# Optimization experiments

Measured on AMD Instinct MI355X. Metric: run time of the kernel, lower is better.

The kernel has to match this reference:

```python
import jax, jax.numpy as jnp
import numpy as np

N_LINEARS = 16
CHANNELS = 3
OUTPUT_DIM = 64
Z_DIM = 128
BATCH = 512


def hash_vectors(z, n):
    # Deterministic surrogate for repo's hash_vectors: map each latent vector
    # to an integer bucket in [0, n). Data-dependent, jit-compatible.
    s = jnp.abs(jnp.sum(z, axis=1)) * 1000.0
    return jnp.mod(jnp.floor(s).astype(jnp.int32), n)


def setup_inputs() -> dict:
    key = jax.random.key(0)
    k1, k2, k3 = jax.random.split(key, 3)
    out_features = CHANNELS * OUTPUT_DIM ** 2 * N_LINEARS  # 196608
    z = jax.random.normal(k1, (BATCH, Z_DIM), dtype=jnp.float32)
    # Linear weight stored as (out_features, in_features), torch convention.
    W = jax.random.normal(k2, (out_features, Z_DIM), dtype=jnp.float32) * (1.0 / np.sqrt(Z_DIM))
    b = jax.random.normal(k3, (out_features,), dtype=jnp.float32) * 0.01
    return {"z": z, "W": W, "b": b}


def reference(z, W, b):
    B = z.shape[0]
    # Dense GEMM: (B, out_features)
    out = jnp.einsum('bi,oi->bo', z, W) + b
    out = out.reshape(B, N_LINEARS, CHANNELS, OUTPUT_DIM, OUTPUT_DIM)
    c = hash_vectors(z, N_LINEARS)  # (B,) int32 in [0, N_LINEARS)
    # Per-sample gather of one linear's output block.
    return jnp.take_along_axis(out, c[:, None, None, None, None], axis=1)[:, 0]
```

## Files before the change

### kernel.cpp

```cpp
#include <hip/hip_runtime.h>
#include <hip/hip_bf16.h>
#include <math.h>


#define N_LINEARS 16
#define ZD 128
#define BATCH 512
#define BLOCK_OUT 12288
#define STILE 48
#define SLOTS 64
#define ZROWS (ZD + 1)
#define TJ 256

typedef float vf16 __attribute__((ext_vector_type(16)));
typedef vf16 vf16u __attribute__((aligned(16)));

#define LISTS_OFF 16
#define BP_OFF (36864 / 4)
#define ZG_OFF_BYTES 65536

__global__ __launch_bounds__(512) void hash_kernel(
    const float* __restrict__ z, int* __restrict__ counts,
    int* __restrict__ lists, int* __restrict__ bp) {
  __shared__ int cnt[N_LINEARS];
  const int b = threadIdx.x;
  if (b < N_LINEARS) cnt[b] = 0;
  __syncthreads();

  const float* zr = z + b * ZD;
  float r0 = zr[0], r1 = zr[1], r2 = zr[2], r3 = zr[3];
  float r4 = zr[4], r5 = zr[5], r6 = zr[6], r7 = zr[7];
  #pragma unroll
  for (int i = 8; i < ZD; i += 8) {
    r0 += zr[i + 0]; r1 += zr[i + 1]; r2 += zr[i + 2]; r3 += zr[i + 3];
    r4 += zr[i + 4]; r5 += zr[i + 5]; r6 += zr[i + 6]; r7 += zr[i + 7];
  }
  float res = ((r0 + r1) + (r2 + r3)) + ((r4 + r5) + (r6 + r7));
  float v = fabsf(res) * 1000.0f;
  int cb = ((int)floorf(v)) & (N_LINEARS - 1);

  int pos = atomicAdd(&cnt[cb], 1);
  lists[(cb << 9) + pos] = b;
  bp[b] = cb | (pos << 4);

  __syncthreads();
  if (b < N_LINEARS) counts[b] = cnt[b];
}

__global__ __launch_bounds__(128) void gather_kernel(
    const float* __restrict__ z, const int* __restrict__ bp,
    float* __restrict__ zgT) {
  const int b = blockIdx.x;
  const int k = threadIdx.x;
  const int v = bp[b];
  const int cb = v & 15;
  const int pos = v >> 4;
  if (pos < SLOTS)
    zgT[(size_t)cb * (ZROWS * SLOTS) + (size_t)k * SLOTS + pos] = z[b * ZD + k];
}


#define ZLOAD(N0, N1, N2, K1)                                        \
  { const vf16u* zr_ = (const vf16u*)(ztp + (size_t)(K1) * SLOTS);   \
    N0 = zr_[0]; N1 = zr_[1]; N2 = zr_[2]; }

#define ZFMA(C0, C1, C2, WK)                                         \
  { const float wk_ = (WK);                                          \
    vf16 wv_;                                                        \
    _Pragma("unroll") for (int e = 0; e < 16; ++e) wv_[e] = wk_;     \
    acc0 += C0 * wv_; acc1 += C1 * wv_; acc2 += C2 * wv_; }

#define STEP(C0, C1, C2, N0, N1, N2, K1, WK)                         \
  ZLOAD(N0, N1, N2, K1) ZFMA(C0, C1, C2, WK)

__global__ __launch_bounds__(TJ, 3) void gen_main_kernel(
    const float* __restrict__ W, const float* __restrict__ bias,
    float* __restrict__ out, const int* __restrict__ counts,
    const int* __restrict__ lists, const float* __restrict__ zgT) {
  const int c = blockIdx.y;
  const int j = blockIdx.x * TJ + threadIdx.x;
  int n = counts[c];
  n = n > SLOTS ? SLOTS : n;
  if (n == 0) return;

  const size_t row = (size_t)c * BLOCK_OUT + (size_t)j;
  const float4* __restrict__ Wv = (const float4*)(W + row * (size_t)ZD);
  const float bj = bias[row];
  const float* __restrict__ zt = zgT + (size_t)c * (ZROWS * SLOTS);
  const int* __restrict__ lst = lists + (c << 9);

  for (int s0 = 0; s0 < n; s0 += STILE) {
    const int m = n - s0;
    vf16 acc0, acc1, acc2;
    #pragma unroll
    for (int e = 0; e < 16; ++e) { acc0[e] = bj; acc1[e] = bj; acc2[e] = bj; }

    const float* ztp = zt + s0;
    vf16 zA0, zA1, zA2, zB0, zB1, zB2;
    ZLOAD(zA0, zA1, zA2, 0)
    float4 wq  = Wv[0];
    float4 wqn = Wv[1];

    for (int kc = 0; kc < ZD / 4; ++kc) {
      const int k0 = kc * 4;
      STEP(zA0, zA1, zA2, zB0, zB1, zB2, k0 + 1, wq.x)
      STEP(zB0, zB1, zB2, zA0, zA1, zA2, k0 + 2, wq.y)
      STEP(zA0, zA1, zA2, zB0, zB1, zB2, k0 + 3, wq.z)
      STEP(zB0, zB1, zB2, zA0, zA1, zA2, k0 + 4, wq.w)
      wq = wqn;
      const int wi = kc + 2 > 31 ? 31 : kc + 2;
      wqn = Wv[wi];
    }

    #pragma unroll
    for (int t = 0; t < 16; ++t)
      if (t < m) out[(size_t)lst[s0 + t] * BLOCK_OUT + j] = acc0[t];
    #pragma unroll
    for (int t = 0; t < 16; ++t)
      if (16 + t < m) out[(size_t)lst[s0 + 16 + t] * BLOCK_OUT + j] = acc1[t];
    #pragma unroll
    for (int t = 0; t < 16; ++t)
      if (32 + t < m) out[(size_t)lst[s0 + 32 + t] * BLOCK_OUT + j] = acc2[t];
  }
}

extern "C" void kernel_launch(void* const* d_in, const int* in_sizes, int n_in,
                              void* d_out, int out_size, void* d_ws, size_t ws_size,
                              hipStream_t stream) {
  const float* z    = (const float*)d_in[0];
  const float* W    = (const float*)d_in[1];
  const float* bias = (const float*)d_in[2];
  float* out = (float*)d_out;

  int*   counts = (int*)d_ws;
  int*   lists  = (int*)d_ws + LISTS_OFF;
  int*   bp     = (int*)d_ws + BP_OFF;
  float* zgT    = (float*)((char*)d_ws + ZG_OFF_BYTES);

  hipLaunchKernelGGL(hash_kernel, dim3(1), dim3(BATCH), 0, stream,
                     z, counts, lists, bp);
  hipLaunchKernelGGL(gather_kernel, dim3(BATCH), dim3(ZD), 0, stream,
                     z, bp, zgT);

  dim3 grid(BLOCK_OUT / TJ, N_LINEARS);
  hipLaunchKernelGGL(gen_main_kernel, grid, dim3(TJ), 0, stream,
                     W, bias, out, counts, lists, zgT);
}
```

Measured before the change: 201.3 us.

## Stage gathered z tile in LDS and specialize tile width by sample count

The gathered, transposed z block and the sample list for each linear are now copied into shared memory once per workgroup, and the inner loop reads z from LDS instead of global memory. Each sample tile is dispatched to a templated body that keeps 1, 2 or 3 accumulator vectors, so tiles with few samples skip wasted FMAs and loads on padded slots. The hash kernel also switches to float4 loads. In exchange each block uses about 33 KB of LDS plus a barrier, which may lower occupancy, and the three template variants enlarge the code.

New measurement: 206.1 us. 2.4% more time.

```diff
diff --git a/kernel.cpp b/kernel.cpp
--- a/kernel.cpp
+++ b/kernel.cpp
@@ -27,13 +27,15 @@
   if (b < N_LINEARS) cnt[b] = 0;
   __syncthreads();
 
-  const float* zr = z + b * ZD;
-  float r0 = zr[0], r1 = zr[1], r2 = zr[2], r3 = zr[3];
-  float r4 = zr[4], r5 = zr[5], r6 = zr[6], r7 = zr[7];
+  const float4* zr4 = (const float4*)(z + b * ZD);
+  const float4 pa = zr4[0], pb = zr4[1];
+  float r0 = pa.x, r1 = pa.y, r2 = pa.z, r3 = pa.w;
+  float r4 = pb.x, r5 = pb.y, r6 = pb.z, r7 = pb.w;
   #pragma unroll
-  for (int i = 8; i < ZD; i += 8) {
-    r0 += zr[i + 0]; r1 += zr[i + 1]; r2 += zr[i + 2]; r3 += zr[i + 3];
-    r4 += zr[i + 4]; r5 += zr[i + 5]; r6 += zr[i + 6]; r7 += zr[i + 7];
+  for (int i = 2; i < ZD / 4; i += 2) {
+    const float4 a = zr4[i], d = zr4[i + 1];
+    r0 += a.x; r1 += a.y; r2 += a.z; r3 += a.w;
+    r4 += d.x; r5 += d.y; r6 += d.z; r7 += d.w;
   }
   float res = ((r0 + r1) + (r2 + r3)) + ((r4 + r5) + (r6 + r7));
   float v = fabsf(res) * 1000.0f;
@@ -60,67 +62,102 @@
 }
 
 
-#define ZLOAD(N0, N1, N2, K1)                                        \
-  { const vf16u* zr_ = (const vf16u*)(ztp + (size_t)(K1) * SLOTS);   \
-    N0 = zr_[0]; N1 = zr_[1]; N2 = zr_[2]; }
+#define ZL(N0, N1, N2, K1)                                           \
+  { const vf16u* zr_ = (const vf16u*)(zp + (K1) * SLOTS);            \
+    N0 = zr_[0];                                                     \
+    if constexpr (NV >= 2) N1 = zr_[1];                              \
+    if constexpr (NV >= 3) N2 = zr_[2]; }
 
-#define ZFMA(C0, C1, C2, WK)                                         \
+#define ZF(C0, C1, C2, WK)                                           \
   { const float wk_ = (WK);                                          \
     vf16 wv_;                                                        \
     _Pragma("unroll") for (int e = 0; e < 16; ++e) wv_[e] = wk_;     \
-    acc0 += C0 * wv_; acc1 += C1 * wv_; acc2 += C2 * wv_; }
+    acc0 += C0 * wv_;                                                \
+    if constexpr (NV >= 2) acc1 += C1 * wv_;                         \
+    if constexpr (NV >= 3) acc2 += C2 * wv_; }
 
 #define STEP(C0, C1, C2, N0, N1, N2, K1, WK)                         \
-  ZLOAD(N0, N1, N2, K1) ZFMA(C0, C1, C2, WK)
+  ZL(N0, N1, N2, K1) ZF(C0, C1, C2, WK)
+
+template <int NV>
+__device__ __forceinline__ void tile_body(
+    const float* __restrict__ zp,
+    const float4* __restrict__ Wv, float bj,
+    float* __restrict__ out, const int* lst, int m, int j) {
+  vf16 acc0, acc1, acc2;
+  _Pragma("unroll") for (int e = 0; e < 16; ++e) acc0[e] = bj;
+  if constexpr (NV >= 2) {
+    _Pragma("unroll") for (int e = 0; e < 16; ++e) acc1[e] = bj;
+  }
+  if constexpr (NV >= 3) {
+    _Pragma("unroll") for (int e = 0; e < 16; ++e) acc2[e] = bj;
+  }
+
+  vf16 zA0, zA1, zA2, zB0, zB1, zB2;
+  ZL(zA0, zA1, zA2, 0)
+  float4 wq  = Wv[0];
+  float4 wqn = Wv[1];
+
+  for (int kc = 0; kc < ZD / 4; ++kc) {
+    const int k0 = kc * 4;
+    STEP(zA0, zA1, zA2, zB0, zB1, zB2, k0 + 1, wq.x)
+    STEP(zB0, zB1, zB2, zA0, zA1, zA2, k0 + 2, wq.y)
+    STEP(zA0, zA1, zA2, zB0, zB1, zB2, k0 + 3, wq.z)
+    STEP(zB0, zB1, zB2, zA0, zA1, zA2, k0 + 4, wq.w)
+    wq = wqn;
+    const int wi = kc + 2 > 31 ? 31 : kc + 2;
+    wqn = Wv[wi];
+  }
+
+  _Pragma("unroll") for (int t = 0; t < 16; ++t)
+    if (t < m) out[(size_t)lst[t] * BLOCK_OUT + j] = acc0[t];
+  if constexpr (NV >= 2) {
+    _Pragma("unroll") for (int t = 0; t < 16; ++t)
+      if (16 + t < m) out[(size_t)lst[16 + t] * BLOCK_OUT + j] = acc1[t];
+  }
+  if constexpr (NV >= 3) {
+    _Pragma("unroll") for (int t = 0; t < 16; ++t)
+      if (32 + t < m) out[(size_t)lst[32 + t] * BLOCK_OUT + j] = acc2[t];
+  }
+}
 
 __global__ __launch_bounds__(TJ, 3) void gen_main_kernel(
     const float* __restrict__ W, const float* __restrict__ bias,
     float* __restrict__ out, const int* __restrict__ counts,
     const int* __restrict__ lists, const float* __restrict__ zgT) {
+  __shared__ float zsh[ZROWS * SLOTS];
+  __shared__ int   lsh[SLOTS];
   const int c = blockIdx.y;
   const int j = blockIdx.x * TJ + threadIdx.x;
   int n = counts[c];
   n = n > SLOTS ? SLOTS : n;
   if (n == 0) return;
 
+  {
+    const float4* zg4 = (const float4*)(zgT + (size_t)c * (ZROWS * SLOTS));
+    float4* ls4 = (float4*)zsh;
+    #pragma unroll
+    for (int i = 0; i < 9; ++i) {
+      const int idx = threadIdx.x + i * TJ;
+      if (idx < (ZROWS * SLOTS) / 4) ls4[idx] = zg4[idx];
+    }
+    if (threadIdx.x < SLOTS) lsh[threadIdx.x] = lists[(c << 9) + threadIdx.x];
+  }
+  __syncthreads();
+
   const size_t row = (size_t)c * BLOCK_OUT + (size_t)j;
   const float4* __restrict__ Wv = (const float4*)(W + row * (size_t)ZD);
   const float bj = bias[row];
-  const float* __restrict__ zt = zgT + (size_t)c * (ZROWS * SLOTS);
-  const int* __restrict__ lst = lists + (c << 9);
 
   for (int s0 = 0; s0 < n; s0 += STILE) {
-    const int m = n - s0;
-    vf16 acc0, acc1, acc2;
-    #pragma unroll
-    for (int e = 0; e < 16; ++e) { acc0[e] = bj; acc1[e] = bj; acc2[e] = bj; }
-
-    const float* ztp = zt + s0;
-    vf16 zA0, zA1, zA2, zB0, zB1, zB2;
-    ZLOAD(zA0, zA1, zA2, 0)
-    float4 wq  = Wv[0];
-    float4 wqn = Wv[1];
-
-    for (int kc = 0; kc < ZD / 4; ++kc) {
-      const int k0 = kc * 4;
-      STEP(zA0, zA1, zA2, zB0, zB1, zB2, k0 + 1, wq.x)
-      STEP(zB0, zB1, zB2, zA0, zA1, zA2, k0 + 2, wq.y)
-      STEP(zA0, zA1, zA2, zB0, zB1, zB2, k0 + 3, wq.z)
-      STEP(zB0, zB1, zB2, zA0, zA1, zA2, k0 + 4, wq.w)
-      wq = wqn;
-      const int wi = kc + 2 > 31 ? 31 : kc + 2;
-      wqn = Wv[wi];
-    }
-
-    #pragma unroll
-    for (int t = 0; t < 16; ++t)
-      if (t < m) out[(size_t)lst[s0 + t] * BLOCK_OUT + j] = acc0[t];
-    #pragma unroll
-    for (int t = 0; t < 16; ++t)
-      if (16 + t < m) out[(size_t)lst[s0 + 16 + t] * BLOCK_OUT + j] = acc1[t];
-    #pragma unroll
-    for (int t = 0; t < 16; ++t)
-      if (32 + t < m) out[(size_t)lst[s0 + 32 + t] * BLOCK_OUT + j] = acc2[t];
+    const int mm = n - s0;
+    const int m = mm > STILE ? STILE : mm;
+    if (m <= 16)
+      tile_body<1>(zsh + s0, Wv, bj, out, lsh + s0, m, j);
+    else if (m <= 32)
+      tile_body<2>(zsh + s0, Wv, bj, out, lsh + s0, m, j);
+    else
+      tile_body<3>(zsh + s0, Wv, bj, out, lsh + s0, m, j);
   }
 }
 
```
